# Performance work log

Hardware: AMD Instinct MI355X
Metric: run time of the kernel (lower is better)

The kernel has to match this reference:

```python
import jax, jax.numpy as jnp
import numpy as np

B, A, NBH, F, G, H = 8, 512, 64, 128, 50, 8
DH = F // H
CUTOFF = 5.0


def setup_inputs() -> dict:
    key = jax.random.key(0)
    ks = jax.random.split(key, 13)
    x = jax.random.normal(ks[0], (B, A, F), jnp.float32)
    e = jax.random.normal(ks[1], (B, A, F), jnp.float32)
    t = jax.random.normal(ks[2], (B, F), jnp.float32)
    # distances in [0, 1.2*cutoff] so some pairs fall outside the cutoff
    r_ij = jax.random.uniform(ks[3], (B, A, NBH), jnp.float32) * (1.2 * CUTOFF)
    f_ij = jax.random.normal(ks[4], (B, A, NBH, G), jnp.float32)
    neighbors = jax.random.randint(ks[5], (B, A, NBH), 0, A, jnp.int32)
    neighbor_mask = jax.random.randint(ks[6], (B, A, NBH), 0, 2, jnp.int32).astype(bool)
    sF = 1.0 / np.sqrt(F).astype(np.float32)
    W_filt = jax.random.normal(ks[7], (G, F), jnp.float32) * (1.0 / np.sqrt(G).astype(np.float32))
    b_filt = jnp.zeros((F,), jnp.float32)
    Wq = jax.random.normal(ks[8], (F, F), jnp.float32) * sF
    Wk = jax.random.normal(ks[9], (F, F), jnp.float32) * sF
    Wv = jax.random.normal(ks[10], (F, F), jnp.float32) * sF
    Wo = jax.random.normal(ks[11], (F, F), jnp.float32) * sF
    bo = jnp.zeros((F,), jnp.float32)
    return dict(e=e, x=x, t=t, r_ij=r_ij, f_ij=f_ij,
                W_filt=W_filt, b_filt=b_filt, Wq=Wq, Wk=Wk, Wv=Wv, Wo=Wo, bo=bo,
                neighbors=neighbors, neighbor_mask=neighbor_mask)


def reference(e, x, t, r_ij, f_ij, W_filt, b_filt, Wq, Wk, Wv, Wo, bo,
              neighbors, neighbor_mask):
    # ---- filter network + cosine cutoff: W (B, A, NBH, F) ----
    W = f_ij @ W_filt + b_filt
    C = 0.5 * (jnp.cos(jnp.pi * r_ij / CUTOFF) + 1.0)
    C = C * (r_ij < CUTOFF).astype(x.dtype)           # (B, A, NBH)
    W = W * C[..., None]

    # ---- neighbor gather: nbh (B, A, NBH, F) ----
    bidx = jnp.arange(B)[:, None, None]
    nbh = x[bidx, neighbors]                           # irregular gather
    nbh = nbh * W                                      # filter-modulated messages

    # ---- EgoAttention: central atom queries its neighbors ----
    q = (x @ Wq).reshape(B, A, H, DH)                  # bahd
    k = (nbh @ Wk).reshape(B, A, NBH, H, DH)           # banhd
    v = (nbh @ Wv).reshape(B, A, NBH, H, DH)
    scale = np.float32(1.0 / np.sqrt(DH))
    scores = jnp.einsum('bahd,banhd->bahn', q, k) * scale
    scores = jnp.where(neighbor_mask[:, :, None, :], scores, jnp.float32(-1e9))
    attn = jax.nn.softmax(scores, axis=-1)             # over neighbors
    msg = jnp.einsum('bahn,banhd->bahd', attn, v).reshape(B, A, F)
    v_out = msg @ Wo + bo

    # ---- residual (apply_transition_function=False branch) ----
    return x + v_out
```

## Files before the change

kernel.cpp:

```cpp
#include <hip/hip_runtime.h>
#include <math.h>

#define BB 8
#define AA 512
#define NBH 64
#define FF 128
#define GG 50
#define CUTOFF 5.0f

typedef __attribute__((ext_vector_type(8)))  short bf16x8;
typedef __attribute__((ext_vector_type(4)))  float f32x4;
typedef __attribute__((ext_vector_type(16))) float f32x16;

#define MST 136

#define WKV_ELEMS (4*8*64*8)
#define WQO_ELEMS (8*4*64*8)
#define WF_ELEMS  (4*4*64*8)

__device__ __forceinline__ short f2bf(float f) {
    union { float f; unsigned u; } v; v.f = f;
    unsigned r = v.u + 0x7fffu + ((v.u >> 16) & 1u);
    return (short)(r >> 16);
}

__device__ __forceinline__ int swz(int n) { return ((n >> 3) & 3) << 3; }

__device__ __forceinline__ bf16x8 ld_f8_bf(const float* p) {
    const float2* p2 = (const float2*)p;
    float2 a = p2[0], b = p2[1], c = p2[2], d = p2[3];
    bf16x8 r;
    r[0] = f2bf(a.x); r[1] = f2bf(a.y); r[2] = f2bf(b.x); r[3] = f2bf(b.y);
    r[4] = f2bf(c.x); r[5] = f2bf(c.y); r[6] = f2bf(d.x); r[7] = f2bf(d.y);
    return r;
}

__device__ __forceinline__ float row16_sum(float x) {
    int t;
    t = __builtin_amdgcn_update_dpp(0, __float_as_int(x), 0x128, 0xf, 0xf, true); x += __int_as_float(t);
    t = __builtin_amdgcn_update_dpp(0, __float_as_int(x), 0x124, 0xf, 0xf, true); x += __int_as_float(t);
    t = __builtin_amdgcn_update_dpp(0, __float_as_int(x), 0x122, 0xf, 0xf, true); x += __int_as_float(t);
    t = __builtin_amdgcn_update_dpp(0, __float_as_int(x), 0x121, 0xf, 0xf, true); x += __int_as_float(t);
    return x;
}

__global__ void prep_kernel(const float* __restrict__ Wk,
                            const float* __restrict__ Wv,
                            const float* __restrict__ Wq,
                            const float* __restrict__ Wo,
                            const float* __restrict__ Wf,
                            short* __restrict__ ws)
{
    int gid = blockIdx.x * blockDim.x + threadIdx.x;
    if (gid < 2 * WKV_ELEMS) {
        const float* src = (gid < WKV_ELEMS) ? Wk : Wv;
        int idx = gid & (WKV_ELEMS - 1);
        int j = idx & 7, l = (idx >> 3) & 63, rest = idx >> 9;
        int s = rest & 7, w = rest >> 3;
        int k = 16 * s + ((l >> 5) << 3) + j;
        int n = 32 * w + (l & 31);
        ws[gid] = f2bf(src[k * FF + n]);
    } else if (gid < 2 * WKV_ELEMS + 2 * WQO_ELEMS) {
        int idx2 = gid - 2 * WKV_ELEMS;
        const float* src = (idx2 < WQO_ELEMS) ? Wq : Wo;
        int idx = idx2 & (WQO_ELEMS - 1);
        int j = idx & 7, l = (idx >> 3) & 63, rest = idx >> 9;
        int s = rest & 3, c = rest >> 2;
        int k = 32 * s + (l >> 4) * 8 + j;
        int n = 16 * c + (l & 15);
        ws[gid] = f2bf(src[k * FF + n]);
    } else {
        int idx = gid - 2 * WKV_ELEMS - 2 * WQO_ELEMS;
        int j = idx & 7, l = (idx >> 3) & 63, rest = idx >> 9;
        int s = rest & 3, w = rest >> 2;
        int k = 16 * s + ((l >> 5) << 3) + j;
        int n = 32 * w + (l & 31);
        ws[gid] = (k < GG) ? f2bf(Wf[k * FF + n]) : (short)0;
    }
}

__global__ __launch_bounds__(256, 4)
void tdt_main(const float* __restrict__ x,
              const float* __restrict__ r_ij,
              const float* __restrict__ f_ij,
              const float* __restrict__ b_filt,
              const float* __restrict__ bo,
              const int*   __restrict__ neighbors,
              const int*   __restrict__ nmask,
              const short* __restrict__ WkB,
              const short* __restrict__ WvB,
              const short* __restrict__ WqB,
              const short* __restrict__ WoB,
              const short* __restrict__ WfB,
              float* __restrict__ out)
{
    const int ba   = blockIdx.x;
    const int b    = ba >> 9;
    const int tid  = threadIdx.x;
    const int lane = tid & 63;
    const int w    = tid >> 6;
    const int l15  = lane & 15;
    const int quad = lane >> 4;
    const int l31  = lane & 31;
    const int khalf = (lane >> 5) << 3;
    const int w5_4  = (lane >> 5) * 4;

    __shared__ short M_s[NBH * MST];
    __shared__ short msg_bf[FF];

    const float* xrow = x + (size_t)ba * FF;
    const float* xb   = x + (size_t)b * AA * FF;
    const size_t bao  = (size_t)ba;

    int   nbr_reg = neighbors[bao * NBH + lane];
    float C_reg;
    {
        float r = r_ij[bao * NBH + lane];
        float c = 0.5f * (__cosf((float)M_PI * r * (1.0f / CUTOFF)) + 1.0f);
        C_reg = (r < CUTOFF) ? c : 0.0f;
    }
    unsigned long long mask64 = __ballot(nmask[bao * NBH + lane] != 0);

    float qvm;
    {
        float qv0, qv1;
#pragma unroll
        for (int ct = 0; ct < 2; ++ct) {
            int cg = 2 * w + ct;
            f32x4 z = {0.f, 0.f, 0.f, 0.f};
#pragma unroll
            for (int s = 0; s < 4; ++s) {
                bf16x8 xa = ld_f8_bf(xrow + 32 * s + quad * 8);
                bf16x8 bq = *(const bf16x8*)&WqB[((cg * 4 + s) * 64 + lane) * 8];
                z = __builtin_amdgcn_mfma_f32_16x16x32_bf16(xa, bq, z, 0, 0, 0);
            }
            if (ct == 0) qv0 = z[0]; else qv1 = z[0];
        }
        qvm = ((lane >> 4) & 1) ? qv1 : qv0;
    }

    {
        f32x16 wacc[2];
#pragma unroll
        for (int mt = 0; mt < 2; ++mt)
#pragma unroll
            for (int r = 0; r < 16; ++r) wacc[mt][r] = 0.0f;

        const float* fm0 = f_ij + bao * (size_t)(NBH * GG) + (size_t)l31 * GG;
#pragma unroll
        for (int s = 0; s < 4; ++s) {
            bf16x8 bfw = *(const bf16x8*)&WfB[((w * 4 + s) * 64 + lane) * 8];
#pragma unroll
            for (int mt = 0; mt < 2; ++mt) {
                const float* fm = fm0 + mt * 32 * GG;
                bf16x8 fa;
                if (s < 3) {
                    fa = ld_f8_bf(fm + 16 * s + khalf);
                } else {
#pragma unroll
                    for (int jj = 0; jj < 8; ++jj) fa[jj] = 0;
                    if (lane < 32) { fa[0] = f2bf(fm[48]); fa[1] = f2bf(fm[49]); }
                }
                wacc[mt] = __builtin_amdgcn_mfma_f32_32x32x16_bf16(fa, bfw, wacc[mt], 0, 0, 0);
            }
        }

        int   c    = 32 * w + l31;
        float bflt = b_filt[c];
#pragma unroll
        for (int mt = 0; mt < 2; ++mt) {
#pragma unroll
            for (int r = 0; r < 16; ++r) {
                int   n   = 32 * mt + (r & 3) + 8 * (r >> 2) + w5_4;
                int   nbn = __shfl(nbr_reg, n, 64);
                float cn  = __shfl(C_reg, n, 64);
                float xv  = xb[(size_t)nbn * FF + c];
                M_s[n * MST + (c ^ swz(n))] = f2bf((wacc[mt][r] + bflt) * cn * xv);
            }
        }
    }
    __syncthreads();

    float sc[2][16];
    float inv;
    {
        f32x16 kacc[2];
#pragma unroll
        for (int mt = 0; mt < 2; ++mt)
#pragma unroll
            for (int r = 0; r < 16; ++r) kacc[mt][r] = 0.0f;
#pragma unroll
        for (int s = 0; s < 8; ++s) {
            bf16x8 bk = *(const bf16x8*)&WkB[((w * 8 + s) * 64 + lane) * 8];
            int kb = 16 * s + khalf;
#pragma unroll
            for (int mt = 0; mt < 2; ++mt) {
                int m = 32 * mt + l31;
                bf16x8 ma = *(const bf16x8*)&M_s[m * MST + (kb ^ swz(m))];
                kacc[mt] = __builtin_amdgcn_mfma_f32_32x32x16_bf16(ma, bk, kacc[mt], 0, 0, 0);
            }
        }
#pragma unroll
        for (int mt = 0; mt < 2; ++mt) {
#pragma unroll
            for (int r = 0; r < 16; ++r) {
                float s = row16_sum(kacc[mt][r] * qvm) * 0.25f;
                int n = 32 * mt + (r & 3) + 8 * (r >> 2) + w5_4;
                sc[mt][r] = ((mask64 >> n) & 1ull) ? s : -1e9f;
            }
        }
        float mx = -1e30f;
#pragma unroll
        for (int mt = 0; mt < 2; ++mt)
#pragma unroll
            for (int r = 0; r < 16; ++r) mx = fmaxf(mx, sc[mt][r]);
        mx = fmaxf(mx, __shfl_xor(mx, 32, 64));
        float sum = 0.0f;
#pragma unroll
        for (int mt = 0; mt < 2; ++mt)
#pragma unroll
            for (int r = 0; r < 16; ++r) {
                float e = __expf(sc[mt][r] - mx);
                sc[mt][r] = e;
                sum += e;
            }
        sum += __shfl_xor(sum, 32, 64);
        inv = 1.0f / sum;
    }

    {
        float acc = 0.0f;
#pragma unroll
        for (int mt = 0; mt < 2; ++mt) {
            f32x16 vacc;
#pragma unroll
            for (int r = 0; r < 16; ++r) vacc[r] = 0.0f;
            int m = 32 * mt + l31;
#pragma unroll
            for (int s = 0; s < 8; ++s) {
                bf16x8 bv = *(const bf16x8*)&WvB[((w * 8 + s) * 64 + lane) * 8];
                int kb = 16 * s + khalf;
                bf16x8 ma = *(const bf16x8*)&M_s[m * MST + (kb ^ swz(m))];
                vacc = __builtin_amdgcn_mfma_f32_32x32x16_bf16(ma, bv, vacc, 0, 0, 0);
            }
#pragma unroll
            for (int r = 0; r < 16; ++r)
                acc = fmaf(sc[mt][r], vacc[r], acc);
        }
        acc += __shfl_xor(acc, 32, 64);
        if (lane < 32) msg_bf[32 * w + l31] = f2bf(acc * inv);
    }
    __syncthreads();

    {
        bf16x8 mga[4];
#pragma unroll
        for (int s = 0; s < 4; ++s)
            mga[s] = *(const bf16x8*)&msg_bf[s * 32 + quad * 8];
#pragma unroll
        for (int ct = 0; ct < 2; ++ct) {
            int cg = 2 * w + ct;
            f32x4 z = {0.f, 0.f, 0.f, 0.f};
#pragma unroll
            for (int s = 0; s < 4; ++s) {
                bf16x8 bw = *(const bf16x8*)&WoB[((cg * 4 + s) * 64 + lane) * 8];
                z = __builtin_amdgcn_mfma_f32_16x16x32_bf16(mga[s], bw, z, 0, 0, 0);
            }
            if (quad == 0) {
                int col = cg * 16 + l15;
                out[bao * FF + col] = z[0] + xrow[col] + bo[col];
            }
        }
    }
}

extern "C" void kernel_launch(void* const* d_in, const int* in_sizes, int n_in,
                              void* d_out, int out_size, void* d_ws, size_t ws_size,
                              hipStream_t stream) {
    const float* x      = (const float*)d_in[1];
    const float* r_ij   = (const float*)d_in[3];
    const float* f_ij   = (const float*)d_in[4];
    const float* W_filt = (const float*)d_in[5];
    const float* b_filt = (const float*)d_in[6];
    const float* Wq     = (const float*)d_in[7];
    const float* Wk     = (const float*)d_in[8];
    const float* Wv     = (const float*)d_in[9];
    const float* Wo     = (const float*)d_in[10];
    const float* bo     = (const float*)d_in[11];
    const int*   nbr    = (const int*)d_in[12];
    const int*   msk    = (const int*)d_in[13];
    float* out = (float*)d_out;

    short* ws  = (short*)d_ws;
    short* WkB = ws;
    short* WvB = ws + WKV_ELEMS;
    short* WqB = ws + 2 * WKV_ELEMS;
    short* WoB = ws + 2 * WKV_ELEMS + WQO_ELEMS;
    short* WfB = ws + 2 * WKV_ELEMS + 2 * WQO_ELEMS;

    int prep_total = 2 * WKV_ELEMS + 2 * WQO_ELEMS + WF_ELEMS;
    hipLaunchKernelGGL(prep_kernel, dim3(prep_total / 256), dim3(256), 0, stream,
                       Wk, Wv, Wq, Wo, W_filt, ws);
    hipLaunchKernelGGL(tdt_main, dim3(BB * AA), dim3(256), 0, stream,
                       x, r_ij, f_ij, b_filt, bo, nbr, msk,
                       WkB, WvB, WqB, WoB, WfB, out);
}
```

Baseline: 164.0 us.

## Fold query into Wk per head so scores come from one MFMA pass

Instead of computing K = M·Wk for every neighbor and then reducing against q with DPP row sums, each block first forms kq = Wk·q_h per head (scaled) in fp32 from the raw Wk, stores it as bf16 in shared memory, and computes scores directly as M·kq with MFMA. This removes the per-neighbor K projection's reduction step and the Wk preconversion in the prep kernel. The bf16 conversions are also switched to a cheaper round-half-up packed form using perm instructions, and the x loads for the q projection are hoisted out of the loop. The exchange is an extra per-block fp32 dot-product stage with global Wk reads, plus slightly different rounding.

```diff
diff --git a/kernel.cpp b/kernel.cpp
--- a/kernel.cpp
+++ b/kernel.cpp
@@ -14,7 +14,7 @@
 
 #define MST 136
 
-#define WKV_ELEMS (4*8*64*8)
+#define WV_ELEMS  (4*8*64*8)
 #define WQO_ELEMS (8*4*64*8)
 #define WF_ELEMS  (4*4*64*8)
 
@@ -23,45 +23,47 @@
     unsigned r = v.u + 0x7fffu + ((v.u >> 16) & 1u);
     return (short)(r >> 16);
 }
-
-__device__ __forceinline__ int swz(int n) { return ((n >> 3) & 3) << 3; }
-
-__device__ __forceinline__ bf16x8 ld_f8_bf(const float* p) {
+__device__ __forceinline__ short f2bf_fast(float f) {
+    return (short)((__float_as_uint(f) + 0x8000u) >> 16);
+}
+__device__ __forceinline__ unsigned int pk2bf(float a, float b) {
+    unsigned int ua = __float_as_uint(a) + 0x8000u;
+    unsigned int ub = __float_as_uint(b) + 0x8000u;
+    return __builtin_amdgcn_perm(ub, ua, 0x07060302u);
+}
+__device__ __forceinline__ bf16x8 ld_f8_bfpk(const float* p) {
     const float2* p2 = (const float2*)p;
     float2 a = p2[0], b = p2[1], c = p2[2], d = p2[3];
-    bf16x8 r;
-    r[0] = f2bf(a.x); r[1] = f2bf(a.y); r[2] = f2bf(b.x); r[3] = f2bf(b.y);
-    r[4] = f2bf(c.x); r[5] = f2bf(c.y); r[6] = f2bf(d.x); r[7] = f2bf(d.y);
-    return r;
-}
-
-__device__ __forceinline__ float row16_sum(float x) {
-    int t;
-    t = __builtin_amdgcn_update_dpp(0, __float_as_int(x), 0x128, 0xf, 0xf, true); x += __int_as_float(t);
-    t = __builtin_amdgcn_update_dpp(0, __float_as_int(x), 0x124, 0xf, 0xf, true); x += __int_as_float(t);
-    t = __builtin_amdgcn_update_dpp(0, __float_as_int(x), 0x122, 0xf, 0xf, true); x += __int_as_float(t);
-    t = __builtin_amdgcn_update_dpp(0, __float_as_int(x), 0x121, 0xf, 0xf, true); x += __int_as_float(t);
-    return x;
-}
-
-__global__ void prep_kernel(const float* __restrict__ Wk,
-                            const float* __restrict__ Wv,
+    union { unsigned int u[4]; bf16x8 v; } r;
+    r.u[0] = pk2bf(a.x, a.y);
+    r.u[1] = pk2bf(b.x, b.y);
+    r.u[2] = pk2bf(c.x, c.y);
+    r.u[3] = pk2bf(d.x, d.y);
+    return r.v;
+}
+__device__ __forceinline__ int swz(int n) { return ((n >> 3) & 3) << 3; }
+__device__ __forceinline__ float dot4(float4 a, float4 b, float acc) {
+    acc = fmaf(a.x, b.x, acc); acc = fmaf(a.y, b.y, acc);
+    acc = fmaf(a.z, b.z, acc); acc = fmaf(a.w, b.w, acc);
+    return acc;
+}
+
+__global__ void prep_kernel(const float* __restrict__ Wv,
                             const float* __restrict__ Wq,
                             const float* __restrict__ Wo,
                             const float* __restrict__ Wf,
                             short* __restrict__ ws)
 {
     int gid = blockIdx.x * blockDim.x + threadIdx.x;
-    if (gid < 2 * WKV_ELEMS) {
-        const float* src = (gid < WKV_ELEMS) ? Wk : Wv;
-        int idx = gid & (WKV_ELEMS - 1);
+    if (gid < WV_ELEMS) {
+        int idx = gid;
         int j = idx & 7, l = (idx >> 3) & 63, rest = idx >> 9;
         int s = rest & 7, w = rest >> 3;
         int k = 16 * s + ((l >> 5) << 3) + j;
         int n = 32 * w + (l & 31);
-        ws[gid] = f2bf(src[k * FF + n]);
-    } else if (gid < 2 * WKV_ELEMS + 2 * WQO_ELEMS) {
-        int idx2 = gid - 2 * WKV_ELEMS;
+        ws[gid] = f2bf(Wv[k * FF + n]);
+    } else if (gid < WV_ELEMS + 2 * WQO_ELEMS) {
+        int idx2 = gid - WV_ELEMS;
         const float* src = (idx2 < WQO_ELEMS) ? Wq : Wo;
         int idx = idx2 & (WQO_ELEMS - 1);
         int j = idx & 7, l = (idx >> 3) & 63, rest = idx >> 9;
@@ -70,7 +72,7 @@
         int n = 16 * c + (l & 15);
         ws[gid] = f2bf(src[k * FF + n]);
     } else {
-        int idx = gid - 2 * WKV_ELEMS - 2 * WQO_ELEMS;
+        int idx = gid - WV_ELEMS - 2 * WQO_ELEMS;
         int j = idx & 7, l = (idx >> 3) & 63, rest = idx >> 9;
         int s = rest & 3, w = rest >> 2;
         int k = 16 * s + ((l >> 5) << 3) + j;
@@ -87,7 +89,7 @@
               const float* __restrict__ bo,
               const int*   __restrict__ neighbors,
               const int*   __restrict__ nmask,
-              const short* __restrict__ WkB,
+              const float* __restrict__ Wk,
               const short* __restrict__ WvB,
               const short* __restrict__ WqB,
               const short* __restrict__ WoB,
@@ -106,6 +108,8 @@
     const int w5_4  = (lane >> 5) * 4;
 
     __shared__ short M_s[NBH * MST];
+    __shared__ float q_s[FF];
+    __shared__ short kq_s[4 * 256];
     __shared__ short msg_bf[FF];
 
     const float* xrow = x + (size_t)ba * FF;
@@ -121,22 +125,22 @@
     }
     unsigned long long mask64 = __ballot(nmask[bao * NBH + lane] != 0);
 
-    float qvm;
-    {
-        float qv0, qv1;
+    {
+        bf16x8 xa[4];
+#pragma unroll
+        for (int s = 0; s < 4; ++s)
+            xa[s] = ld_f8_bfpk(xrow + 32 * s + quad * 8);
 #pragma unroll
         for (int ct = 0; ct < 2; ++ct) {
             int cg = 2 * w + ct;
             f32x4 z = {0.f, 0.f, 0.f, 0.f};
 #pragma unroll
             for (int s = 0; s < 4; ++s) {
-                bf16x8 xa = ld_f8_bf(xrow + 32 * s + quad * 8);
                 bf16x8 bq = *(const bf16x8*)&WqB[((cg * 4 + s) * 64 + lane) * 8];
-                z = __builtin_amdgcn_mfma_f32_16x16x32_bf16(xa, bq, z, 0, 0, 0);
-            }
-            if (ct == 0) qv0 = z[0]; else qv1 = z[0];
-        }
-        qvm = ((lane >> 4) & 1) ? qv1 : qv0;
+                z = __builtin_amdgcn_mfma_f32_16x16x32_bf16(xa[s], bq, z, 0, 0, 0);
+            }
+            if (quad == 0) q_s[cg * 16 + l15] = z[0];
+        }
     }
 
     {
@@ -155,11 +159,11 @@
                 const float* fm = fm0 + mt * 32 * GG;
                 bf16x8 fa;
                 if (s < 3) {
-                    fa = ld_f8_bf(fm + 16 * s + khalf);
+                    fa = ld_f8_bfpk(fm + 16 * s + khalf);
                 } else {
 #pragma unroll
                     for (int jj = 0; jj < 8; ++jj) fa[jj] = 0;
-                    if (lane < 32) { fa[0] = f2bf(fm[48]); fa[1] = f2bf(fm[49]); }
+                    if (lane < 32) { fa[0] = f2bf_fast(fm[48]); fa[1] = f2bf_fast(fm[49]); }
                 }
                 wacc[mt] = __builtin_amdgcn_mfma_f32_32x32x16_bf16(fa, bfw, wacc[mt], 0, 0, 0);
             }
@@ -175,53 +179,73 @@
                 int   nbn = __shfl(nbr_reg, n, 64);
                 float cn  = __shfl(C_reg, n, 64);
                 float xv  = xb[(size_t)nbn * FF + c];
-                M_s[n * MST + (c ^ swz(n))] = f2bf((wacc[mt][r] + bflt) * cn * xv);
+                M_s[n * MST + (c ^ swz(n))] = f2bf_fast((wacc[mt][r] + bflt) * cn * xv);
             }
         }
     }
     __syncthreads();
 
-    float sc[2][16];
-    float inv;
-    {
-        f32x16 kacc[2];
-#pragma unroll
-        for (int mt = 0; mt < 2; ++mt)
-#pragma unroll
-            for (int r = 0; r < 16; ++r) kacc[mt][r] = 0.0f;
+    f32x16 sc2[2];
+#pragma unroll
+    for (int mt = 0; mt < 2; ++mt)
+#pragma unroll
+        for (int r = 0; r < 16; ++r) sc2[mt][r] = 0.0f;
+    {
+        const int hloc = lane >> 5;
+        const int head = 2 * w + hloc;
+        const int i0   = (lane & 31) * 4;
+        const float4* qv4 = (const float4*)&q_s[w * 32 + hloc * 16];
+        float4 qA = qv4[0], qB = qv4[1], qC = qv4[2], qD = qv4[3];
+        float kqv[4];
+#pragma unroll
+        for (int p = 0; p < 4; ++p) {
+            const float4* wr = (const float4*)&Wk[(size_t)(i0 + p) * FF + head * 16];
+            float acc = dot4(wr[0], qA, 0.0f);
+            acc = dot4(wr[1], qB, acc);
+            acc = dot4(wr[2], qC, acc);
+            acc = dot4(wr[3], qD, acc);
+            kqv[p] = acc * 0.25f;
+        }
+        uint2 pk;
+        pk.x = pk2bf(kqv[0], kqv[1]);
+        pk.y = pk2bf(kqv[2], kqv[3]);
+        *(uint2*)&kq_s[w * 256 + hloc * 128 + i0] = pk;
+    }
+    {
+        const short* kqbase = &kq_s[w * 256 + (l31 >> 4) * 128];
 #pragma unroll
         for (int s = 0; s < 8; ++s) {
-            bf16x8 bk = *(const bf16x8*)&WkB[((w * 8 + s) * 64 + lane) * 8];
-            int kb = 16 * s + khalf;
+            bf16x8 bkq = *(const bf16x8*)&kqbase[16 * s + khalf];
 #pragma unroll
             for (int mt = 0; mt < 2; ++mt) {
                 int m = 32 * mt + l31;
-                bf16x8 ma = *(const bf16x8*)&M_s[m * MST + (kb ^ swz(m))];
-                kacc[mt] = __builtin_amdgcn_mfma_f32_32x32x16_bf16(ma, bk, kacc[mt], 0, 0, 0);
-            }
-        }
-#pragma unroll
-        for (int mt = 0; mt < 2; ++mt) {
+                bf16x8 ma = *(const bf16x8*)&M_s[m * MST + ((16 * s + khalf) ^ swz(m))];
+                sc2[mt] = __builtin_amdgcn_mfma_f32_32x32x16_bf16(ma, bkq, sc2[mt], 0, 0, 0);
+            }
+        }
+    }
+    float inv;
+    {
+#pragma unroll
+        for (int mt = 0; mt < 2; ++mt)
 #pragma unroll
             for (int r = 0; r < 16; ++r) {
-                float s = row16_sum(kacc[mt][r] * qvm) * 0.25f;
                 int n = 32 * mt + (r & 3) + 8 * (r >> 2) + w5_4;
-                sc[mt][r] = ((mask64 >> n) & 1ull) ? s : -1e9f;
-            }
-        }
+                if (!((mask64 >> n) & 1ull)) sc2[mt][r] = -1e9f;
+            }
         float mx = -1e30f;
 #pragma unroll
         for (int mt = 0; mt < 2; ++mt)
 #pragma unroll
-            for (int r = 0; r < 16; ++r) mx = fmaxf(mx, sc[mt][r]);
+            for (int r = 0; r < 16; ++r) mx = fmaxf(mx, sc2[mt][r]);
         mx = fmaxf(mx, __shfl_xor(mx, 32, 64));
         float sum = 0.0f;
 #pragma unroll
         for (int mt = 0; mt < 2; ++mt)
 #pragma unroll
             for (int r = 0; r < 16; ++r) {
-                float e = __expf(sc[mt][r] - mx);
-                sc[mt][r] = e;
+                float e = __expf(sc2[mt][r] - mx);
+                sc2[mt][r] = e;
                 sum += e;
             }
         sum += __shfl_xor(sum, 32, 64);
@@ -245,10 +269,10 @@
             }
 #pragma unroll
             for (int r = 0; r < 16; ++r)
-                acc = fmaf(sc[mt][r], vacc[r], acc);
+                acc = fmaf(sc2[mt][r], vacc[r], acc);
         }
         acc += __shfl_xor(acc, 32, 64);
-        if (lane < 32) msg_bf[32 * w + l31] = f2bf(acc * inv);
+        if (lane < 32) msg_bf[32 * w + l31] = f2bf_fast(acc * inv);
     }
     __syncthreads();
 
@@ -292,16 +316,15 @@
     float* out = (float*)d_out;
 
     short* ws  = (short*)d_ws;
-    short* WkB = ws;
-    short* WvB = ws + WKV_ELEMS;
-    short* WqB = ws + 2 * WKV_ELEMS;
-    short* WoB = ws + 2 * WKV_ELEMS + WQO_ELEMS;
-    short* WfB = ws + 2 * WKV_ELEMS + 2 * WQO_ELEMS;
-
-    int prep_total = 2 * WKV_ELEMS + 2 * WQO_ELEMS + WF_ELEMS;
+    short* WvB = ws;
+    short* WqB = ws + WV_ELEMS;
+    short* WoB = ws + WV_ELEMS + WQO_ELEMS;
+    short* WfB = ws + WV_ELEMS + 2 * WQO_ELEMS;
+
+    int prep_total = WV_ELEMS + 2 * WQO_ELEMS + WF_ELEMS;
     hipLaunchKernelGGL(prep_kernel, dim3(prep_total / 256), dim3(256), 0, stream,
-                       Wk, Wv, Wq, Wo, W_filt, ws);
+                       Wv, Wq, Wo, W_filt, ws);
     hipLaunchKernelGGL(tdt_main, dim3(BB * AA), dim3(256), 0, stream,
                        x, r_ij, f_ij, b_filt, bo, nbr, msk,
-                       WkB, WvB, WqB, WoB, WfB, out);
-}
+                       Wk, WvB, WqB, WoB, WfB, out);
+}
```

After: 185.8 us. 13.3% more time.
